# Optimization experiments

Measured on AMD Instinct MI355X. Metric: run time of the kernel, lower is better.

## Reference

```python
import jax, jax.numpy as jnp
import numpy as np

H = 8          # n_heads
THRESH = 0.5   # edge pruning threshold
LN_EPS = 1e-5


def setup_inputs() -> dict:
    key = jax.random.key(0)
    ks = jax.random.split(key, 24)
    B, S, D = 8, 128, 256
    N = S + 1
    hd = D // H

    def lin(k, fan_in, fan_out, gain=1.0):
        # xavier_uniform-ish init, stored as [in, out] (y = x @ W + b)
        lim = gain * np.sqrt(6.0 / (fan_in + fan_out))
        return jax.random.uniform(k, (fan_in, fan_out), jnp.float32, -lim, lim)

    g = 1.0 / np.sqrt(2.0)
    return {
        "desc": jax.random.normal(ks[0], (B, S, D), jnp.float32),
        "nv": jax.random.normal(ks[1], (B, N, D), jnp.float32),
        "W_gt": lin(ks[2], D, D), "b_gt": jnp.zeros((D,), jnp.float32),
        "topo_bias": jnp.zeros((1,), jnp.float32),
        "W_q": lin(ks[3], D, D, g), "b_q": jnp.zeros((D,), jnp.float32),
        "W_k": lin(ks[4], D, D, g), "b_k": jnp.zeros((D,), jnp.float32),
        "W_v": lin(ks[5], D, D, g), "b_v": jnp.zeros((D,), jnp.float32),
        "W_e1": lin(ks[6], 2 * D, D), "b_e1": jnp.zeros((D,), jnp.float32),
        "ln_g": jnp.ones((D,), jnp.float32), "ln_b": jnp.zeros((D,), jnp.float32),
        "W_e2": lin(ks[7], D, D), "b_e2": jnp.zeros((D,), jnp.float32),
        "w_attn": lin(ks[8], 3 * hd, 1, g)[:, 0], "b_attn": jnp.zeros((), jnp.float32),
        "W_o": lin(ks[9], D, D, g), "b_o": jnp.zeros((D,), jnp.float32),
    }


def _forward(desc, nv, W_gt, b_gt, topo_bias, W_q, b_q, W_k, b_k, W_v, b_v,
             W_e1, b_e1, ln_g, ln_b, W_e2, b_e2, w_attn, b_attn, W_o, b_o):
    B, N, D = nv.shape
    S = N - 1
    hd = D // H

    # 1. global topology
    d = desc @ W_gt + b_gt                                   # [B,S,D]
    dn = d / jnp.linalg.norm(d, axis=-1, keepdims=True)
    global_top = jax.nn.sigmoid(jnp.einsum('bid,bjd->bij', dn, dn) + topo_bias[0])

    # 2. sample-wise similarity
    var = nv[:, 1:, :]
    vn = var / jnp.linalg.norm(var, axis=-1, keepdims=True)
    sample_sim = jnp.einsum('bid,bjd->bij', vn, vn)
    adj_mat = global_top * sample_sim

    # 3. remove self-connection, squash
    diag_mask = 1.0 - jnp.eye(S, dtype=adj_mat.dtype)
    adj = jax.nn.sigmoid(adj_mat * diag_mask)

    # 4. straight-through edge pruning (frozen=False path)
    hard = (adj > THRESH).astype(adj.dtype)
    adj = hard - jax.lax.stop_gradient(adj) + adj

    # 5. edge attributes: Linear(concat(d_i,d_j)) decomposed into two matmuls
    a = d @ W_e1[:D]                                          # node_i part [B,S,D]
    b_ = d @ W_e1[D:]                                         # node_j part [B,S,D]
    pre = jnp.zeros((B, N, N, D), dtype=d.dtype)
    pre = pre.at[:, 1:, 1:].set(a[:, :, None, :] + b_[:, None, :, :])
    cls = a + b_                                              # concat(d_j,d_j) rows
    pre = pre.at[:, 0, 1:].set(cls).at[:, 1:, 0].set(cls)
    pre = pre + b_e1                                          # (0,0) entry = bias only (zeros input)
    mu = pre.mean(-1, keepdims=True)
    vr = ((pre - mu) ** 2).mean(-1, keepdims=True)
    e = jax.nn.relu((pre - mu) * jax.lax.rsqrt(vr + LN_EPS) * ln_g + ln_b)
    e = e @ W_e2 + b_e2                                       # [B,N,N,D]
    e = e.reshape(B, N, N, H, hd).transpose(0, 3, 1, 2, 4)    # [B,H,N,N,hd]

    # padded adjacency: CLS row attends to all vars, col 0 masked
    na = jnp.zeros((B, N, N), dtype=adj.dtype)
    na = na.at[:, 1:, 1:].set(adj).at[:, 0, 1:].set(1.0)
    e = e * na[:, None, :, :, None]

    # 6. additive attention: attn_proj(concat(q,k,e)) decomposed
    q = (nv @ W_q + b_q).reshape(B, N, H, hd).transpose(0, 2, 1, 3)
    k = (nv @ W_k + b_k).reshape(B, N, H, hd).transpose(0, 2, 1, 3)
    v = (nv @ W_v + b_v).reshape(B, N, H, hd).transpose(0, 2, 1, 3)
    wq, wk, we = w_attn[:hd], w_attn[hd:2 * hd], w_attn[2 * hd:]
    scores = (jnp.einsum('bhid,d->bhi', q, wq)[:, :, :, None]
              + jnp.einsum('bhjd,d->bhj', k, wk)[:, :, None, :]
              + jnp.einsum('bhijd,d->bhij', e, we) + b_attn)
    scores = scores + (na[:, None, :, :] == 0).astype(scores.dtype) * -1e9
    attn = jax.nn.softmax(scores, axis=-1)                    # dropout = identity (eval)

    ctx = jnp.einsum('bhij,bhjd->bhid', attn, v)
    out = ctx.transpose(0, 2, 1, 3).reshape(B, N, D) @ W_o + b_o
    return out, attn


def reference(desc, nv, W_gt, b_gt, topo_bias, W_q, b_q, W_k, b_k, W_v, b_v,
              W_e1, b_e1, ln_g, ln_b, W_e2, b_e2, w_attn, b_attn, W_o, b_o):
    return _forward(desc, nv, W_gt, b_gt, topo_bias, W_q, b_q, W_k, b_k, W_v, b_v,
                    W_e1, b_e1, ln_g, ln_b, W_e2, b_e2, w_attn, b_attn, W_o, b_o)
```

## Files before the change

### kernel.cpp

```cpp
#include <hip/hip_runtime.h>
#include <math.h>

#define BB 8
#define SS 128
#define NN 129
#define DD 256
#define HH 8
#define LN_EPS 1e-5f

#define OFF_A    0
#define OFF_BPT  262144
#define OFF_CPT  524288
#define OFF_VART 786432
#define OFF_V    1048576
#define OFF_SQ   1312768
#define OFF_SK   1321024
#define OFF_MA   1329280
#define OFF_QA   1330304
#define OFF_MB   1331328
#define OFF_QB   1332352
#define OFF_MC   1333376
#define OFF_QC   1334400
#define OFF_U    1335424
#define OFF_UB   1337472

struct SA {
    float dsc[4][DD];
    float drow[4][DD];
    float4 red[8][4][64];
    float part[24][4];
};
struct SB {
    float rows[2][DD];
    float4 redq[8][2][64];
    float4 redk[8][2][64];
};
union SMA { SA a; SB b; };

__global__ __launch_bounds__(512) void ka_all(
    const float* __restrict__ desc, const float* __restrict__ nv,
    const float* __restrict__ W_gt, const float* __restrict__ b_gt,
    const float* __restrict__ W_e1, const float* __restrict__ b_e1,
    const float* __restrict__ W_q, const float* __restrict__ b_q,
    const float* __restrict__ W_k, const float* __restrict__ b_k,
    const float* __restrict__ W_v, const float* __restrict__ b_v,
    const float* __restrict__ W_e2, const float* __restrict__ b_e2,
    const float* __restrict__ w_attn,
    float* __restrict__ a, float* __restrict__ bp_t, float* __restrict__ cp_t,
    float* __restrict__ var_t, float* __restrict__ v,
    float* __restrict__ sq, float* __restrict__ sk,
    float* __restrict__ ma, float* __restrict__ qa, float* __restrict__ mb,
    float* __restrict__ qb, float* __restrict__ mc, float* __restrict__ qc,
    float* __restrict__ U, float* __restrict__ ubias) {
    __shared__ SMA sm;
    const int bx = blockIdx.x, t = threadIdx.x;

    if (bx < 256) {
        SA& S = sm.a;
        const int b = bx >> 5, s0 = (bx & 31) * 4;
        const int dq = t & 63, kh = t >> 6;
        for (int e = t; e < 4 * DD; e += 512)
            S.dsc[e >> 8][e & 255] = desc[(size_t)(b * SS + s0 + (e >> 8)) * DD + (e & 255)];
        __syncthreads();
        {
            float4 acc[4];
#pragma unroll
            for (int r = 0; r < 4; r++) acc[r] = make_float4(0.f, 0.f, 0.f, 0.f);
            const int kb = kh * 32;
#pragma unroll 4
            for (int k = kb; k < kb + 32; k++) {
                float4 w = *(const float4*)&W_gt[k * DD + 4 * dq];
#pragma unroll
                for (int r = 0; r < 4; r++) {
                    float x = S.dsc[r][k];
                    acc[r].x = fmaf(x, w.x, acc[r].x); acc[r].y = fmaf(x, w.y, acc[r].y);
                    acc[r].z = fmaf(x, w.z, acc[r].z); acc[r].w = fmaf(x, w.w, acc[r].w);
                }
            }
#pragma unroll
            for (int r = 0; r < 4; r++) S.red[kh][r][dq] = acc[r];
        }
        __syncthreads();
        for (int e = t; e < 4 * DD; e += 512) {
            int r = e >> 8, d2 = e & 255;
            float s = b_gt[d2];
#pragma unroll
            for (int kk = 0; kk < 8; kk++) s += ((const float*)S.red[kk][r])[d2];
            S.drow[r][d2] = s;
        }
        __syncthreads();
        {
            float4 acc[4];
#pragma unroll
            for (int r = 0; r < 4; r++) acc[r] = make_float4(0.f, 0.f, 0.f, 0.f);
            const int kb = kh * 32;
#pragma unroll 4
            for (int k = kb; k < kb + 32; k++) {
                float4 w = *(const float4*)&W_e1[k * DD + 4 * dq];
#pragma unroll
                for (int r = 0; r < 4; r++) {
                    float x = S.drow[r][k];
                    acc[r].x = fmaf(x, w.x, acc[r].x); acc[r].y = fmaf(x, w.y, acc[r].y);
                    acc[r].z = fmaf(x, w.z, acc[r].z); acc[r].w = fmaf(x, w.w, acc[r].w);
                }
            }
#pragma unroll
            for (int r = 0; r < 4; r++) S.red[kh][r][dq] = acc[r];
        }
        __syncthreads();
        float avf[4];
        if (t < 256) {
            const int d2 = t;
#pragma unroll
            for (int r = 0; r < 4; r++) {
                float s = 0.f;
#pragma unroll
                for (int kk = 0; kk < 8; kk++) s += ((const float*)S.red[kk][r])[d2];
                avf[r] = s;
                a[(size_t)(b * SS + s0 + r) * DD + d2] = s;
            }
        }
        __syncthreads();
        {
            float4 acc[4];
#pragma unroll
            for (int r = 0; r < 4; r++) acc[r] = make_float4(0.f, 0.f, 0.f, 0.f);
            const int kb = kh * 32;
#pragma unroll 4
            for (int k = kb; k < kb + 32; k++) {
                float4 w = *(const float4*)&W_e1[(DD + k) * DD + 4 * dq];
#pragma unroll
                for (int r = 0; r < 4; r++) {
                    float x = S.drow[r][k];
                    acc[r].x = fmaf(x, w.x, acc[r].x); acc[r].y = fmaf(x, w.y, acc[r].y);
                    acc[r].z = fmaf(x, w.z, acc[r].z); acc[r].w = fmaf(x, w.w, acc[r].w);
                }
            }
#pragma unroll
            for (int r = 0; r < 4; r++) S.red[kh][r][dq] = acc[r];
        }
        __syncthreads();
        if (t < 256) {
            const int d2 = t;
            float bvf[4], cvf[4];
            float be1 = b_e1[d2];
#pragma unroll
            for (int r = 0; r < 4; r++) {
                float s = 0.f;
#pragma unroll
                for (int kk = 0; kk < 8; kk++) s += ((const float*)S.red[kk][r])[d2];
                bvf[r] = s + be1; cvf[r] = avf[r] + bvf[r];
            }
            float4 f4;
            f4.x = bvf[0]; f4.y = bvf[1]; f4.z = bvf[2]; f4.w = bvf[3];
            *(float4*)(bp_t + (size_t)(b * DD + d2) * SS + s0) = f4;
            f4.x = cvf[0]; f4.y = cvf[1]; f4.z = cvf[2]; f4.w = cvf[3];
            *(float4*)(cp_t + (size_t)(b * DD + d2) * SS + s0) = f4;
            float nvv[4];
#pragma unroll
            for (int r = 0; r < 4; r++) nvv[r] = nv[(size_t)(b * NN + 1 + s0 + r) * DD + d2];
            f4.x = nvv[0]; f4.y = nvv[1]; f4.z = nvv[2]; f4.w = nvv[3];
            *(float4*)(var_t + (size_t)(b * DD + d2) * SS + s0) = f4;
            float vals[24];
#pragma unroll
            for (int r = 0; r < 4; r++) {
                vals[r * 6 + 0] = avf[r]; vals[r * 6 + 1] = avf[r] * avf[r];
                vals[r * 6 + 2] = bvf[r]; vals[r * 6 + 3] = bvf[r] * bvf[r];
                vals[r * 6 + 4] = cvf[r]; vals[r * 6 + 5] = cvf[r] * cvf[r];
            }
            int lane = t & 63, wid = t >> 6;
#pragma unroll
            for (int vv = 0; vv < 24; vv++) {
                float x = vals[vv];
                for (int o = 32; o; o >>= 1) x += __shfl_xor(x, o, 64);
                if (lane == 0) S.part[vv][wid] = x;
            }
        }
        __syncthreads();
        if (t < 24) {
            float ssum = (S.part[t][0] + S.part[t][1]) + (S.part[t][2] + S.part[t][3]);
            int st = t % 6;
            int row = b * SS + s0 + t / 6;
            float m = ssum * (1.f / DD);
            float* dstp = (st == 0) ? ma : (st == 1) ? qa : (st == 2) ? mb
                         : (st == 3) ? qb : (st == 4) ? mc : qc;
            dstp[row] = m;
        }
    } else if (bx < 776) {
        SB& S = sm.b;
        const int idx = bx - 256;
        const int b = idx / 65, n0 = (idx % 65) * 2;
        const int dq = t & 63, kh = t >> 6;
        {
            int r = t >> 8, d2 = t & 255;
            int n = n0 + r; if (n >= NN) n = NN - 1;
            S.rows[r][d2] = nv[(size_t)(b * NN + n) * DD + d2];
        }
        __syncthreads();
        {
            float4 aq[2], ak[2];
#pragma unroll
            for (int r = 0; r < 2; r++) { aq[r] = make_float4(0.f, 0.f, 0.f, 0.f); ak[r] = aq[r]; }
            const int kb = kh * 32;
#pragma unroll 4
            for (int k = kb; k < kb + 32; k++) {
                float4 wq = *(const float4*)&W_q[k * DD + 4 * dq];
                float4 wk = *(const float4*)&W_k[k * DD + 4 * dq];
#pragma unroll
                for (int r = 0; r < 2; r++) {
                    float x = S.rows[r][k];
                    aq[r].x = fmaf(x, wq.x, aq[r].x); aq[r].y = fmaf(x, wq.y, aq[r].y);
                    aq[r].z = fmaf(x, wq.z, aq[r].z); aq[r].w = fmaf(x, wq.w, aq[r].w);
                    ak[r].x = fmaf(x, wk.x, ak[r].x); ak[r].y = fmaf(x, wk.y, ak[r].y);
                    ak[r].z = fmaf(x, wk.z, ak[r].z); ak[r].w = fmaf(x, wk.w, ak[r].w);
                }
            }
#pragma unroll
            for (int r = 0; r < 2; r++) { S.redq[kh][r][dq] = aq[r]; S.redk[kh][r][dq] = ak[r]; }
        }
        __syncthreads();
        {
            const int d2 = t & 255, r = t >> 8;
            const int n = n0 + r;
            float qf = b_q[d2], kf = b_k[d2];
#pragma unroll
            for (int kk = 0; kk < 8; kk++) {
                qf += ((const float*)S.redq[kk][r])[d2];
                kf += ((const float*)S.redk[kk][r])[d2];
            }
            float xq = qf * w_attn[d2 & 31];
            float xk = kf * w_attn[32 + (d2 & 31)];
#pragma unroll
            for (int o = 16; o; o >>= 1) { xq += __shfl_xor(xq, o, 32); xk += __shfl_xor(xk, o, 32); }
            if ((d2 & 31) == 0 && n < NN) {
                sq[(size_t)(b * HH + (d2 >> 5)) * NN + n] = xq;
                sk[(size_t)(b * HH + (d2 >> 5)) * NN + n] = xk;
            }
        }
        __syncthreads();
        {
            float4 av[2];
#pragma unroll
            for (int r = 0; r < 2; r++) av[r] = make_float4(0.f, 0.f, 0.f, 0.f);
            const int kb = kh * 32;
#pragma unroll 4
            for (int k = kb; k < kb + 32; k++) {
                float4 wv = *(const float4*)&W_v[k * DD + 4 * dq];
#pragma unroll
                for (int r = 0; r < 2; r++) {
                    float x = S.rows[r][k];
                    av[r].x = fmaf(x, wv.x, av[r].x); av[r].y = fmaf(x, wv.y, av[r].y);
                    av[r].z = fmaf(x, wv.z, av[r].z); av[r].w = fmaf(x, wv.w, av[r].w);
                }
            }
#pragma unroll
            for (int r = 0; r < 2; r++) S.redq[kh][r][dq] = av[r];
        }
        __syncthreads();
        {
            const int d2 = t & 255, r = t >> 8;
            const int n = n0 + r;
            if (n < NN) {
                float vf = b_v[d2];
#pragma unroll
                for (int kk = 0; kk < 8; kk++) vf += ((const float*)S.redq[kk][r])[d2];
                v[(size_t)(b * NN + n) * DD + d2] = vf;
            }
        }
    } else {
        const int ri = bx - 776;
        if (t < 256) {
            const int c = t;
            const float wec = w_attn[64 + (c & 31)];
#pragma unroll
            for (int rr = 0; rr < 4; rr++) {
                int r = ri * 4 + rr;
                float x = W_e2[(size_t)r * DD + c] * wec;
#pragma unroll
                for (int o = 16; o; o >>= 1) x += __shfl_xor(x, o, 32);
                if ((c & 31) == 0) U[r * HH + (c >> 5)] = x;
            }
            if (ri == 0) {
                float x = b_e2[c] * wec;
#pragma unroll
                for (int o = 16; o; o >>= 1) x += __shfl_xor(x, o, 32);
                if ((c & 31) == 0) ubias[c >> 5] = x;
            }
        }
    }
}

__global__ __launch_bounds__(256) void kmega4(
    const float* __restrict__ a, const float* __restrict__ bp_t, const float* __restrict__ cp_t,
    const float* __restrict__ var_t, const float* __restrict__ nv,
    const float* __restrict__ v,
    const float* __restrict__ ma, const float* __restrict__ qa,
    const float* __restrict__ mb, const float* __restrict__ qb,
    const float* __restrict__ mc, const float* __restrict__ qc,
    const float* __restrict__ sq, const float* __restrict__ sk,
    const float* __restrict__ ln_g, const float* __restrict__ ln_b,
    const float* __restrict__ U, const float* __restrict__ ubias,
    const float* __restrict__ b_attn,
    const float* __restrict__ W_o, const float* __restrict__ b_o,
    float* __restrict__ attn, float* __restrict__ out) {
    const int i = blockIdx.x, b = blockIdx.y;
    const int t = threadIdx.x;
    const int w = t >> 6, l = t & 63;
    const int dgp = l >> 4;
    const int jp = w * 16 + (l & 15);

    __shared__ float Arow[DD];
    __shared__ __attribute__((aligned(8))) float2 lnsm[DD];
    __shared__ __attribute__((aligned(16))) float4 Usm[DD][2];
    __shared__ __attribute__((aligned(8))) float rsm[SS], nmm[SS], mkm[SS], pnm[SS];
    __shared__ float skm[HH * NN];
    __shared__ float sqb[HH], ubm[HH];
    __shared__ float sc[HH][NN + 3];
    __shared__ union { float Vrow[DD]; float csm[DD]; } uv;
    __shared__ __attribute__((aligned(16))) union {
        struct { float crs[SS]; float dvs[SS]; } p1;
        float redc[4][DD];
    } ur;

    {
        Arow[t] = (i >= 1) ? a[((size_t)b * SS + i - 1) * DD + t] : 0.f;
        uv.Vrow[t] = nv[((size_t)b * NN + i) * DD + t];
        float2 g; g.x = ln_g[t]; g.y = ln_b[t]; lnsm[t] = g;
        Usm[t][0] = *(const float4*)&U[t * HH];
        Usm[t][1] = *(const float4*)&U[t * HH + 4];
        for (int e = t; e < HH * NN; e += 256) skm[e] = sk[(size_t)b * HH * NN + e];
        if (t < HH) {
            sqb[t] = sq[(size_t)b * HH * NN + t * NN + i] + b_attn[0];
            ubm[t] = ubias[t];
        }
    }
    __syncthreads();

    if (i >= 1) {
        float cr[2] = {0.f, 0.f}, dvv[2] = {0.f, 0.f};
        const float* bc = bp_t + ((size_t)b * DD + dgp * 64) * SS + 2 * jp;
        const float* vc = var_t + ((size_t)b * DD + dgp * 64) * SS + 2 * jp;
#pragma unroll 8
        for (int dd = 0; dd < 64; dd++) {
            float2 bv = *(const float2*)(bc + (size_t)dd * SS);
            float2 vv = *(const float2*)(vc + (size_t)dd * SS);
            const int d = dgp * 64 + dd;
            float A0 = Arow[d], V0 = uv.Vrow[d];
            cr[0] = fmaf(A0, bv.x, cr[0]); cr[1] = fmaf(A0, bv.y, cr[1]);
            dvv[0] = fmaf(V0, vv.x, dvv[0]); dvv[1] = fmaf(V0, vv.y, dvv[1]);
        }
#pragma unroll
        for (int jj = 0; jj < 2; jj++) {
            float c = cr[jj], d2 = dvv[jj];
            c += __shfl_xor(c, 16); c += __shfl_xor(c, 32);
            d2 += __shfl_xor(d2, 16); d2 += __shfl_xor(d2, 32);
            cr[jj] = c; dvv[jj] = d2;
        }
        if (l < 16) {
            float2 wc; wc.x = cr[0]; wc.y = cr[1];
            float2 wd; wd.x = dvv[0]; wd.y = dvv[1];
            *(float2*)&ur.p1.crs[2 * jp] = wc;
            *(float2*)&ur.p1.dvs[2 * jp] = wd;
        }
    }
    __syncthreads();
    if (t < SS) {
        const int j = t;
        float rs, nm, mk, pen;
        if (i == 0) {
            float mu = mc[b * SS + j], q2 = qc[b * SS + j];
            rs = rsqrtf(q2 - mu * mu + LN_EPS); nm = -mu * rs; mk = 1.f; pen = 0.f;
        } else {
            float cr = ur.p1.crs[j];
            float dv = ur.p1.dvs[j];
            float muA = ma[b * SS + i - 1], qA = qa[b * SS + i - 1];
            float muB = mb[b * SS + j], qB = qb[b * SS + j];
            float mu = muA + muB;
            float var = qA + qB + 2.f * cr * (1.f / DD) - mu * mu;
            rs = rsqrtf(var + LN_EPS); nm = -mu * rs;
            mk = ((i - 1) != j && dv > 0.f) ? 1.f : 0.f;
            pen = (mk == 0.f) ? -1e9f : 0.f;
        }
        rsm[j] = rs; nmm[j] = nm; mkm[j] = mk; pnm[j] = pen;
    }
    __syncthreads();
    float acc[HH][2];
#pragma unroll
    for (int h = 0; h < HH; h++) { acc[h][0] = 0.f; acc[h][1] = 0.f; }
    {
        const float* Bp = ((i == 0) ? cp_t : bp_t) + ((size_t)b * DD + dgp * 64) * SS + 2 * jp;
        float2 r0 = *(const float2*)&rsm[2 * jp];
        float2 n0 = *(const float2*)&nmm[2 * jp];
#pragma unroll 8
        for (int dd = 0; dd < 64; dd++) {
            const int d = dgp * 64 + dd;
            float2 bv = *(const float2*)(Bp + (size_t)dd * SS);
            float A0 = Arow[d];
            float2 gb = lnsm[d];
            float4 u0 = Usm[d][0], u1 = Usm[d][1];
            float y0 = fmaf(A0 + bv.x, r0.x, n0.x); y0 = fmaf(y0, gb.x, gb.y);
            float y1 = fmaf(A0 + bv.y, r0.y, n0.y); y1 = fmaf(y1, gb.x, gb.y);
            float e0 = fmaxf(y0, 0.f), e1 = fmaxf(y1, 0.f);
            acc[0][0] = fmaf(e0, u0.x, acc[0][0]); acc[0][1] = fmaf(e1, u0.x, acc[0][1]);
            acc[1][0] = fmaf(e0, u0.y, acc[1][0]); acc[1][1] = fmaf(e1, u0.y, acc[1][1]);
            acc[2][0] = fmaf(e0, u0.z, acc[2][0]); acc[2][1] = fmaf(e1, u0.z, acc[2][1]);
            acc[3][0] = fmaf(e0, u0.w, acc[3][0]); acc[3][1] = fmaf(e1, u0.w, acc[3][1]);
            acc[4][0] = fmaf(e0, u1.x, acc[4][0]); acc[4][1] = fmaf(e1, u1.x, acc[4][1]);
            acc[5][0] = fmaf(e0, u1.y, acc[5][0]); acc[5][1] = fmaf(e1, u1.y, acc[5][1]);
            acc[6][0] = fmaf(e0, u1.z, acc[6][0]); acc[6][1] = fmaf(e1, u1.z, acc[6][1]);
            acc[7][0] = fmaf(e0, u1.w, acc[7][0]); acc[7][1] = fmaf(e1, u1.w, acc[7][1]);
        }
    }
#pragma unroll
    for (int h = 0; h < HH; h++) {
        float s0 = acc[h][0], s1 = acc[h][1];
        s0 += __shfl_xor(s0, 16); s0 += __shfl_xor(s0, 32);
        s1 += __shfl_xor(s1, 16); s1 += __shfl_xor(s1, 32);
        acc[h][0] = s0; acc[h][1] = s1;
    }
    if (l < 16) {
        const int j0 = 2 * jp, j1 = j0 + 1;
        float mk0 = mkm[j0], pn0 = pnm[j0];
        float mk1 = mkm[j1], pn1 = pnm[j1];
#pragma unroll
        for (int h = 0; h < HH; h++) {
            sc[h][1 + j0] = sqb[h] + skm[h * NN + 1 + j0] + (acc[h][0] + ubm[h]) * mk0 + pn0;
            sc[h][1 + j1] = sqb[h] + skm[h * NN + 1 + j1] + (acc[h][1] + ubm[h]) * mk1 + pn1;
        }
    }
    if (t < HH) sc[t][0] = sqb[t] + skm[t * NN] - 1e9f;
    __syncthreads();
    {
        const int h = t >> 5, ll = t & 31;
        float m = -INFINITY;
        for (int j = ll; j < NN; j += 32) m = fmaxf(m, sc[h][j]);
#pragma unroll
        for (int o = 16; o; o >>= 1) m = fmaxf(m, __shfl_xor(m, o, 32));
        float s = 0.f;
        float ev[5];
        int cnt = 0;
        for (int j = ll; j < NN; j += 32) { float e = __expf(sc[h][j] - m); ev[cnt++] = e; s += e; }
#pragma unroll
        for (int o = 16; o; o >>= 1) s += __shfl_xor(s, o, 32);
        float inv = 1.f / s;
        float* arow = attn + (((size_t)b * HH + h) * NN + i) * NN;
        cnt = 0;
        for (int j = ll; j < NN; j += 32) {
            float p = ev[cnt++] * inv;
            sc[h][j] = p;
            arow[j] = p;
        }
    }
    __syncthreads();
    {
        const int dq = t & 63, jg = t >> 6;
        const int h = dq >> 3;
        float ca[4] = {0.f, 0.f, 0.f, 0.f};
#pragma unroll 8
        for (int jj = 0; jj < 33; jj++) {
            int j = jg * 33 + jj;
            if (j < NN) {
                float4 vv = *(const float4*)&v[((size_t)b * NN + j) * DD + 4 * dq];
                float p0 = sc[h][j];
                ca[0] = fmaf(p0, vv.x, ca[0]); ca[1] = fmaf(p0, vv.y, ca[1]);
                ca[2] = fmaf(p0, vv.z, ca[2]); ca[3] = fmaf(p0, vv.w, ca[3]);
            }
        }
        float4 wv; wv.x = ca[0]; wv.y = ca[1]; wv.z = ca[2]; wv.w = ca[3];
        *(float4*)&ur.redc[jg][4 * dq] = wv;
    }
    __syncthreads();
    uv.csm[t] = (ur.redc[0][t] + ur.redc[1][t]) + (ur.redc[2][t] + ur.redc[3][t]);
    __syncthreads();
    {
        const int cq = t & 63, kg = t >> 6;
        float o[4] = {0.f, 0.f, 0.f, 0.f};
#pragma unroll 8
        for (int kk = 0; kk < 64; kk++) {
            int k = kg * 64 + kk;
            float4 wv = *(const float4*)&W_o[(size_t)k * DD + 4 * cq];
            float c0 = uv.csm[k];
            o[0] = fmaf(c0, wv.x, o[0]); o[1] = fmaf(c0, wv.y, o[1]);
            o[2] = fmaf(c0, wv.z, o[2]); o[3] = fmaf(c0, wv.w, o[3]);
        }
        __syncthreads();
        float4 wv; wv.x = o[0]; wv.y = o[1]; wv.z = o[2]; wv.w = o[3];
        *(float4*)&ur.redc[kg][4 * cq] = wv;
    }
    __syncthreads();
    {
        float s = (ur.redc[0][t] + ur.redc[1][t]) + (ur.redc[2][t] + ur.redc[3][t]) + b_o[t];
        out[((size_t)b * NN + i) * DD + t] = s;
    }
}

extern "C" void kernel_launch(void* const* d_in, const int* in_sizes, int n_in,
                              void* d_out, int out_size, void* d_ws, size_t ws_size,
                              hipStream_t stream) {
    const float* desc   = (const float*)d_in[0];
    const float* nv     = (const float*)d_in[1];
    const float* W_gt   = (const float*)d_in[2];
    const float* b_gt   = (const float*)d_in[3];
    const float* W_q    = (const float*)d_in[5];
    const float* b_q    = (const float*)d_in[6];
    const float* W_k    = (const float*)d_in[7];
    const float* b_k    = (const float*)d_in[8];
    const float* W_v    = (const float*)d_in[9];
    const float* b_v    = (const float*)d_in[10];
    const float* W_e1   = (const float*)d_in[11];
    const float* b_e1   = (const float*)d_in[12];
    const float* ln_g   = (const float*)d_in[13];
    const float* ln_b   = (const float*)d_in[14];
    const float* W_e2   = (const float*)d_in[15];
    const float* b_e2   = (const float*)d_in[16];
    const float* w_attn = (const float*)d_in[17];
    const float* b_attn = (const float*)d_in[18];
    const float* W_o    = (const float*)d_in[19];
    const float* b_o    = (const float*)d_in[20];

    float* ws   = (float*)d_ws;
    float* a    = ws + OFF_A;
    float* bp_t = ws + OFF_BPT;
    float* cp_t = ws + OFF_CPT;
    float* vart = ws + OFF_VART;
    float* v    = ws + OFF_V;
    float* sq   = ws + OFF_SQ;
    float* sk   = ws + OFF_SK;
    float* ma   = ws + OFF_MA;
    float* qa   = ws + OFF_QA;
    float* mb   = ws + OFF_MB;
    float* qb   = ws + OFF_QB;
    float* mc   = ws + OFF_MC;
    float* qc   = ws + OFF_QC;
    float* U    = ws + OFF_U;
    float* ub   = ws + OFF_UB;

    float* out  = (float*)d_out;
    float* attn = (float*)d_out + (size_t)BB * NN * DD;

    ka_all<<<dim3(840), dim3(512), 0, stream>>>(
        desc, nv, W_gt, b_gt, W_e1, b_e1, W_q, b_q, W_k, b_k, W_v, b_v,
        W_e2, b_e2, w_attn,
        a, bp_t, cp_t, vart, v, sq, sk, ma, qa, mb, qb, mc, qc, U, ub);
    kmega4<<<dim3(NN, BB), dim3(256), 0, stream>>>(
        a, bp_t, cp_t, vart, nv, v, ma, qa, mb, qb, mc, qc, sq, sk,
        ln_g, ln_b, U, ub, b_attn, W_o, b_o, attn, out);
}
```

Measured before the change: 178.2 us.

## Process two query rows per block to reuse V and W_o loads

The fused attention kernel now handles two rows i per block (grid 65x8 instead of 129x8). Each wave pair takes one row and splits the D reduction in halves, so the per-row shuffle reductions become shared-memory partial sums. The V and W_o loads in the context and output projections are shared across both rows. The per-row shared staging of A, V, ln params and U is replaced by direct global loads. This halves the block count, which lowers parallelism to 520 blocks, and adds register pressure and extra syncs.

```diff
diff --git a/kernel.cpp b/kernel.cpp
--- a/kernel.cpp
+++ b/kernel.cpp
@@ -290,7 +290,7 @@
     }
 }
 
-__global__ __launch_bounds__(256) void kmega4(
+__global__ __launch_bounds__(256) void kmega5(
     const float* __restrict__ a, const float* __restrict__ bp_t, const float* __restrict__ cp_t,
     const float* __restrict__ var_t, const float* __restrict__ nv,
     const float* __restrict__ v,
@@ -303,103 +303,110 @@
     const float* __restrict__ b_attn,
     const float* __restrict__ W_o, const float* __restrict__ b_o,
     float* __restrict__ attn, float* __restrict__ out) {
-    const int i = blockIdx.x, b = blockIdx.y;
+    const int it = blockIdx.x, b = blockIdx.y;
+    const int i0 = it * 2;
     const int t = threadIdx.x;
-    const int w = t >> 6, l = t & 63;
-    const int dgp = l >> 4;
-    const int jp = w * 16 + (l & 15);
-
-    __shared__ float Arow[DD];
-    __shared__ __attribute__((aligned(8))) float2 lnsm[DD];
-    __shared__ __attribute__((aligned(16))) float4 Usm[DD][2];
-    __shared__ __attribute__((aligned(8))) float rsm[SS], nmm[SS], mkm[SS], pnm[SS];
+    const int w = __builtin_amdgcn_readfirstlane(t >> 6);
+    const int l = t & 63;
+    const int iw = w >> 1;
+    const int dh = w & 1;
+    const int jp = l;
+
+    __shared__ __attribute__((aligned(8))) float rsm[2][SS], nmm[2][SS], mkm[2][SS], pnm[2][SS];
     __shared__ float skm[HH * NN];
-    __shared__ float sqb[HH], ubm[HH];
-    __shared__ float sc[HH][NN + 3];
-    __shared__ union { float Vrow[DD]; float csm[DD]; } uv;
+    __shared__ float sqb[2][HH], ubm[HH];
+    __shared__ float sc[2][HH][NN + 3];
+    __shared__ float csm[2][DD];
     __shared__ __attribute__((aligned(16))) union {
-        struct { float crs[SS]; float dvs[SS]; } p1;
-        float redc[4][DD];
+        struct { float crs[2][2][SS]; float dvs[2][2][SS]; } p1;
+        float red2[2][2][HH][SS];
+        float redc[4][2][DD];
     } ur;
 
+    const int ic = (i0 + iw < NN) ? i0 + iw : NN - 1;
+
     {
-        Arow[t] = (i >= 1) ? a[((size_t)b * SS + i - 1) * DD + t] : 0.f;
-        uv.Vrow[t] = nv[((size_t)b * NN + i) * DD + t];
-        float2 g; g.x = ln_g[t]; g.y = ln_b[t]; lnsm[t] = g;
-        Usm[t][0] = *(const float4*)&U[t * HH];
-        Usm[t][1] = *(const float4*)&U[t * HH + 4];
         for (int e = t; e < HH * NN; e += 256) skm[e] = sk[(size_t)b * HH * NN + e];
-        if (t < HH) {
-            sqb[t] = sq[(size_t)b * HH * NN + t * NN + i] + b_attn[0];
-            ubm[t] = ubias[t];
-        }
-    }
-    __syncthreads();
-
-    if (i >= 1) {
-        float cr[2] = {0.f, 0.f}, dvv[2] = {0.f, 0.f};
-        const float* bc = bp_t + ((size_t)b * DD + dgp * 64) * SS + 2 * jp;
-        const float* vc = var_t + ((size_t)b * DD + dgp * 64) * SS + 2 * jp;
+        if (t < 16) {
+            int il = t >> 3, h = t & 7;
+            int i = i0 + il; if (i > NN - 1) i = NN - 1;
+            sqb[il][h] = sq[(size_t)b * HH * NN + h * NN + i] + b_attn[0];
+        }
+        if (t < HH) ubm[t] = ubias[t];
+    }
+    __syncthreads();
+
+    if (ic >= 1) {
+        const float* __restrict__ Ap = a + ((size_t)b * SS + ic - 1) * DD;
+        const float* __restrict__ Vp = nv + ((size_t)b * NN + ic) * DD;
+        const float* bc = bp_t + ((size_t)b * DD + dh * 128) * SS + 2 * jp;
+        const float* vc = var_t + ((size_t)b * DD + dh * 128) * SS + 2 * jp;
+        float cr0 = 0.f, cr1 = 0.f, dv0 = 0.f, dv1 = 0.f;
 #pragma unroll 8
-        for (int dd = 0; dd < 64; dd++) {
+        for (int dd = 0; dd < 128; dd++) {
+            const int d = dh * 128 + dd;
+            float A = Ap[d];
+            float V = Vp[d];
             float2 bv = *(const float2*)(bc + (size_t)dd * SS);
             float2 vv = *(const float2*)(vc + (size_t)dd * SS);
-            const int d = dgp * 64 + dd;
-            float A0 = Arow[d], V0 = uv.Vrow[d];
-            cr[0] = fmaf(A0, bv.x, cr[0]); cr[1] = fmaf(A0, bv.y, cr[1]);
-            dvv[0] = fmaf(V0, vv.x, dvv[0]); dvv[1] = fmaf(V0, vv.y, dvv[1]);
-        }
-#pragma unroll
-        for (int jj = 0; jj < 2; jj++) {
-            float c = cr[jj], d2 = dvv[jj];
-            c += __shfl_xor(c, 16); c += __shfl_xor(c, 32);
-            d2 += __shfl_xor(d2, 16); d2 += __shfl_xor(d2, 32);
-            cr[jj] = c; dvv[jj] = d2;
-        }
-        if (l < 16) {
-            float2 wc; wc.x = cr[0]; wc.y = cr[1];
-            float2 wd; wd.x = dvv[0]; wd.y = dvv[1];
-            *(float2*)&ur.p1.crs[2 * jp] = wc;
-            *(float2*)&ur.p1.dvs[2 * jp] = wd;
-        }
+            cr0 = fmaf(A, bv.x, cr0); cr1 = fmaf(A, bv.y, cr1);
+            dv0 = fmaf(V, vv.x, dv0); dv1 = fmaf(V, vv.y, dv1);
+        }
+        float2 wc; wc.x = cr0; wc.y = cr1;
+        float2 wd; wd.x = dv0; wd.y = dv1;
+        *(float2*)&ur.p1.crs[iw][dh][2 * jp] = wc;
+        *(float2*)&ur.p1.dvs[iw][dh][2 * jp] = wd;
+    } else {
+        float2 z; z.x = 0.f; z.y = 0.f;
+        *(float2*)&ur.p1.crs[iw][dh][2 * jp] = z;
+        *(float2*)&ur.p1.dvs[iw][dh][2 * jp] = z;
     }
     __syncthreads();
     if (t < SS) {
         const int j = t;
-        float rs, nm, mk, pen;
-        if (i == 0) {
-            float mu = mc[b * SS + j], q2 = qc[b * SS + j];
-            rs = rsqrtf(q2 - mu * mu + LN_EPS); nm = -mu * rs; mk = 1.f; pen = 0.f;
-        } else {
-            float cr = ur.p1.crs[j];
-            float dv = ur.p1.dvs[j];
-            float muA = ma[b * SS + i - 1], qA = qa[b * SS + i - 1];
-            float muB = mb[b * SS + j], qB = qb[b * SS + j];
-            float mu = muA + muB;
-            float var = qA + qB + 2.f * cr * (1.f / DD) - mu * mu;
-            rs = rsqrtf(var + LN_EPS); nm = -mu * rs;
-            mk = ((i - 1) != j && dv > 0.f) ? 1.f : 0.f;
-            pen = (mk == 0.f) ? -1e9f : 0.f;
-        }
-        rsm[j] = rs; nmm[j] = nm; mkm[j] = mk; pnm[j] = pen;
+#pragma unroll
+        for (int il = 0; il < 2; il++) {
+            int i = i0 + il; if (i > NN - 1) i = NN - 1;
+            float rs, nm, mk, pen;
+            if (i == 0) {
+                float mu = mc[b * SS + j], q2 = qc[b * SS + j];
+                rs = rsqrtf(q2 - mu * mu + LN_EPS); nm = -mu * rs; mk = 1.f; pen = 0.f;
+            } else {
+                float cr = ur.p1.crs[il][0][j] + ur.p1.crs[il][1][j];
+                float dv = ur.p1.dvs[il][0][j] + ur.p1.dvs[il][1][j];
+                float muA = ma[b * SS + i - 1], qA = qa[b * SS + i - 1];
+                float muB = mb[b * SS + j], qB = qb[b * SS + j];
+                float mu = muA + muB;
+                float var = qA + qB + 2.f * cr * (1.f / DD) - mu * mu;
+                rs = rsqrtf(var + LN_EPS); nm = -mu * rs;
+                mk = ((i - 1) != j && dv > 0.f) ? 1.f : 0.f;
+                pen = (mk == 0.f) ? -1e9f : 0.f;
+            }
+            rsm[il][j] = rs; nmm[il][j] = nm; mkm[il][j] = mk; pnm[il][j] = pen;
+        }
     }
     __syncthreads();
     float acc[HH][2];
 #pragma unroll
     for (int h = 0; h < HH; h++) { acc[h][0] = 0.f; acc[h][1] = 0.f; }
     {
-        const float* Bp = ((i == 0) ? cp_t : bp_t) + ((size_t)b * DD + dgp * 64) * SS + 2 * jp;
-        float2 r0 = *(const float2*)&rsm[2 * jp];
-        float2 n0 = *(const float2*)&nmm[2 * jp];
+        const bool isI0 = (ic == 0);
+        const float afl = isI0 ? 0.f : 1.f;
+        const float* __restrict__ Ap = a + ((size_t)b * SS + (isI0 ? 0 : ic - 1)) * DD;
+        const float* Bp = (isI0 ? cp_t : bp_t) + ((size_t)b * DD + dh * 128) * SS + 2 * jp;
+        float2 r0 = *(const float2*)&rsm[iw][2 * jp];
+        float2 n0 = *(const float2*)&nmm[iw][2 * jp];
 #pragma unroll 8
-        for (int dd = 0; dd < 64; dd++) {
-            const int d = dgp * 64 + dd;
+        for (int dd = 0; dd < 128; dd++) {
+            const int d = dh * 128 + dd;
+            float A = Ap[d] * afl;
+            float g = ln_g[d];
+            float be = ln_b[d];
+            float4 u0 = *(const float4*)&U[d * HH];
+            float4 u1 = *(const float4*)&U[d * HH + 4];
             float2 bv = *(const float2*)(Bp + (size_t)dd * SS);
-            float A0 = Arow[d];
-            float2 gb = lnsm[d];
-            float4 u0 = Usm[d][0], u1 = Usm[d][1];
-            float y0 = fmaf(A0 + bv.x, r0.x, n0.x); y0 = fmaf(y0, gb.x, gb.y);
-            float y1 = fmaf(A0 + bv.y, r0.y, n0.y); y1 = fmaf(y1, gb.x, gb.y);
+            float y0 = fmaf(A + bv.x, r0.x, n0.x); y0 = fmaf(y0, g, be);
+            float y1 = fmaf(A + bv.y, r0.y, n0.y); y1 = fmaf(y1, g, be);
             float e0 = fmaxf(y0, 0.f), e1 = fmaxf(y1, 0.f);
             acc[0][0] = fmaf(e0, u0.x, acc[0][0]); acc[0][1] = fmaf(e1, u0.x, acc[0][1]);
             acc[1][0] = fmaf(e0, u0.y, acc[1][0]); acc[1][1] = fmaf(e1, u0.y, acc[1][1]);
@@ -411,86 +418,105 @@
             acc[7][0] = fmaf(e0, u1.w, acc[7][0]); acc[7][1] = fmaf(e1, u1.w, acc[7][1]);
         }
     }
+    __syncthreads();
 #pragma unroll
     for (int h = 0; h < HH; h++) {
-        float s0 = acc[h][0], s1 = acc[h][1];
-        s0 += __shfl_xor(s0, 16); s0 += __shfl_xor(s0, 32);
-        s1 += __shfl_xor(s1, 16); s1 += __shfl_xor(s1, 32);
-        acc[h][0] = s0; acc[h][1] = s1;
-    }
-    if (l < 16) {
-        const int j0 = 2 * jp, j1 = j0 + 1;
-        float mk0 = mkm[j0], pn0 = pnm[j0];
-        float mk1 = mkm[j1], pn1 = pnm[j1];
-#pragma unroll
-        for (int h = 0; h < HH; h++) {
-            sc[h][1 + j0] = sqb[h] + skm[h * NN + 1 + j0] + (acc[h][0] + ubm[h]) * mk0 + pn0;
-            sc[h][1 + j1] = sqb[h] + skm[h * NN + 1 + j1] + (acc[h][1] + ubm[h]) * mk1 + pn1;
-        }
-    }
-    if (t < HH) sc[t][0] = sqb[t] + skm[t * NN] - 1e9f;
+        float2 wv; wv.x = acc[h][0]; wv.y = acc[h][1];
+        *(float2*)&ur.red2[iw][dh][h][2 * jp] = wv;
+    }
+    __syncthreads();
+    for (int e = t; e < 2 * HH * SS; e += 256) {
+        int il = e >> 10, h = (e >> 7) & 7, j = e & 127;
+        float s = ur.red2[il][0][h][j] + ur.red2[il][1][h][j];
+        sc[il][h][1 + j] = sqb[il][h] + skm[h * NN + 1 + j] + (s + ubm[h]) * mkm[il][j] + pnm[il][j];
+    }
+    if (t < 16) { int il = t >> 3, h = t & 7; sc[il][h][0] = sqb[il][h] + skm[h * NN] - 1e9f; }
     __syncthreads();
     {
-        const int h = t >> 5, ll = t & 31;
+        const int row = t >> 4, ll = t & 15;
+        const int il = row >> 3, h = row & 7;
+        const int i = i0 + il;
         float m = -INFINITY;
-        for (int j = ll; j < NN; j += 32) m = fmaxf(m, sc[h][j]);
-#pragma unroll
-        for (int o = 16; o; o >>= 1) m = fmaxf(m, __shfl_xor(m, o, 32));
+        for (int j = ll; j < NN; j += 16) m = fmaxf(m, sc[il][h][j]);
+#pragma unroll
+        for (int o = 8; o; o >>= 1) m = fmaxf(m, __shfl_xor(m, o, 16));
         float s = 0.f;
-        float ev[5];
+        float ev[9];
         int cnt = 0;
-        for (int j = ll; j < NN; j += 32) { float e = __expf(sc[h][j] - m); ev[cnt++] = e; s += e; }
-#pragma unroll
-        for (int o = 16; o; o >>= 1) s += __shfl_xor(s, o, 32);
+        for (int j = ll; j < NN; j += 16) { float e = __expf(sc[il][h][j] - m); ev[cnt++] = e; s += e; }
+#pragma unroll
+        for (int o = 8; o; o >>= 1) s += __shfl_xor(s, o, 16);
         float inv = 1.f / s;
         float* arow = attn + (((size_t)b * HH + h) * NN + i) * NN;
         cnt = 0;
-        for (int j = ll; j < NN; j += 32) {
+        for (int j = ll; j < NN; j += 16) {
             float p = ev[cnt++] * inv;
-            sc[h][j] = p;
-            arow[j] = p;
+            sc[il][h][j] = p;
+            if (i < NN) arow[j] = p;
         }
     }
     __syncthreads();
     {
-        const int dq = t & 63, jg = t >> 6;
+        const int dq = t & 63, jg = w;
         const int h = dq >> 3;
-        float ca[4] = {0.f, 0.f, 0.f, 0.f};
+        float ca[2][4] = {{0.f, 0.f, 0.f, 0.f}, {0.f, 0.f, 0.f, 0.f}};
 #pragma unroll 8
         for (int jj = 0; jj < 33; jj++) {
             int j = jg * 33 + jj;
             if (j < NN) {
                 float4 vv = *(const float4*)&v[((size_t)b * NN + j) * DD + 4 * dq];
-                float p0 = sc[h][j];
-                ca[0] = fmaf(p0, vv.x, ca[0]); ca[1] = fmaf(p0, vv.y, ca[1]);
-                ca[2] = fmaf(p0, vv.z, ca[2]); ca[3] = fmaf(p0, vv.w, ca[3]);
-            }
-        }
-        float4 wv; wv.x = ca[0]; wv.y = ca[1]; wv.z = ca[2]; wv.w = ca[3];
-        *(float4*)&ur.redc[jg][4 * dq] = wv;
-    }
-    __syncthreads();
-    uv.csm[t] = (ur.redc[0][t] + ur.redc[1][t]) + (ur.redc[2][t] + ur.redc[3][t]);
+                float p0 = sc[0][h][j], p1 = sc[1][h][j];
+                ca[0][0] = fmaf(p0, vv.x, ca[0][0]); ca[0][1] = fmaf(p0, vv.y, ca[0][1]);
+                ca[0][2] = fmaf(p0, vv.z, ca[0][2]); ca[0][3] = fmaf(p0, vv.w, ca[0][3]);
+                ca[1][0] = fmaf(p1, vv.x, ca[1][0]); ca[1][1] = fmaf(p1, vv.y, ca[1][1]);
+                ca[1][2] = fmaf(p1, vv.z, ca[1][2]); ca[1][3] = fmaf(p1, vv.w, ca[1][3]);
+            }
+        }
+        __syncthreads();
+#pragma unroll
+        for (int il = 0; il < 2; il++) {
+            float4 wv; wv.x = ca[il][0]; wv.y = ca[il][1]; wv.z = ca[il][2]; wv.w = ca[il][3];
+            *(float4*)&ur.redc[jg][il][4 * dq] = wv;
+        }
+    }
+    __syncthreads();
+#pragma unroll
+    for (int il = 0; il < 2; il++)
+        csm[il][t] = (ur.redc[0][il][t] + ur.redc[1][il][t])
+                   + (ur.redc[2][il][t] + ur.redc[3][il][t]);
     __syncthreads();
     {
-        const int cq = t & 63, kg = t >> 6;
-        float o[4] = {0.f, 0.f, 0.f, 0.f};
+        const int cq = t & 63, kg = w;
+        float o[2][4] = {{0.f, 0.f, 0.f, 0.f}, {0.f, 0.f, 0.f, 0.f}};
 #pragma unroll 8
         for (int kk = 0; kk < 64; kk++) {
             int k = kg * 64 + kk;
             float4 wv = *(const float4*)&W_o[(size_t)k * DD + 4 * cq];
-            float c0 = uv.csm[k];
-            o[0] = fmaf(c0, wv.x, o[0]); o[1] = fmaf(c0, wv.y, o[1]);
-            o[2] = fmaf(c0, wv.z, o[2]); o[3] = fmaf(c0, wv.w, o[3]);
-        }
-        __syncthreads();
-        float4 wv; wv.x = o[0]; wv.y = o[1]; wv.z = o[2]; wv.w = o[3];
-        *(float4*)&ur.redc[kg][4 * cq] = wv;
+            float c0 = csm[0][k], c1 = csm[1][k];
+            o[0][0] = fmaf(c0, wv.x, o[0][0]); o[0][1] = fmaf(c0, wv.y, o[0][1]);
+            o[0][2] = fmaf(c0, wv.z, o[0][2]); o[0][3] = fmaf(c0, wv.w, o[0][3]);
+            o[1][0] = fmaf(c1, wv.x, o[1][0]); o[1][1] = fmaf(c1, wv.y, o[1][1]);
+            o[1][2] = fmaf(c1, wv.z, o[1][2]); o[1][3] = fmaf(c1, wv.w, o[1][3]);
+        }
+        __syncthreads();
+#pragma unroll
+        for (int il = 0; il < 2; il++) {
+            float4 wv; wv.x = o[il][0]; wv.y = o[il][1]; wv.z = o[il][2]; wv.w = o[il][3];
+            *(float4*)&ur.redc[kg][il][4 * cq] = wv;
+        }
     }
     __syncthreads();
     {
-        float s = (ur.redc[0][t] + ur.redc[1][t]) + (ur.redc[2][t] + ur.redc[3][t]) + b_o[t];
-        out[((size_t)b * NN + i) * DD + t] = s;
+        float bo = b_o[t];
+#pragma unroll
+        for (int il = 0; il < 2; il++) {
+            int i = i0 + il;
+            if (i < NN) {
+                float s = (ur.redc[0][il][t] + ur.redc[1][il][t])
+                        + (ur.redc[2][il][t] + ur.redc[3][il][t]) + bo;
+                out[((size_t)b * NN + i) * DD + t] = s;
+            }
+        }
     }
 }
 
@@ -542,7 +568,7 @@
         desc, nv, W_gt, b_gt, W_e1, b_e1, W_q, b_q, W_k, b_k, W_v, b_v,
         W_e2, b_e2, w_attn,
         a, bp_t, cp_t, vart, v, sq, sk, ma, qa, mb, qb, mc, qc, U, ub);
-    kmega4<<<dim3(NN, BB), dim3(256), 0, stream>>>(
+    kmega5<<<dim3(65, BB), dim3(256), 0, stream>>>(
         a, bp_t, cp_t, vart, nv, v, ma, qa, mb, qb, mc, qc, sq, sk,
         ln_g, ln_b, U, ub, b_attn, W_o, b_o, attn, out);
 }
```

Result: slower. 181.8 us (+2.0%).
